# Performance work log

Measured on AMD Instinct MI355X. Metric: run time of the kernel, lower is better.

Reference implementation:

```python
import jax, jax.numpy as jnp
import numpy as np

B, CIN, COUT, H, W = 4, 128, 128, 128, 128
K, G, PAD = 3, 4, 1  # kernel_size, deformable_groups, padding=(K-1)//2
CG = CIN // G


def setup_inputs() -> dict:
    key = jax.random.key(0)
    k1, k2, k3, k4 = jax.random.split(key, 4)
    x = jax.random.normal(k1, (B, CIN, H, W), jnp.float32)
    # 1x1 offset conv (in module it is zero-initialized; use small random values
    # so the bilinear-sampling path is actually exercised)
    w_off = jax.random.normal(k2, (G * K * K * 2, CIN), jnp.float32) * 0.01
    b_off = jax.random.normal(k3, (G * K * K * 2,), jnp.float32) * 0.1
    # DeformConv weight [Cout, Cin, K, K] (DCNv1 has no bias)
    w_def = jax.random.normal(k4, (COUT, CIN, K, K), jnp.float32) * (1.0 / np.sqrt(CIN * K * K))
    return {"x": x, "w_off": w_off, "b_off": b_off, "w_def": w_def}


def _deform_conv(x, offset, w):
    """DCNv1: per-location bilinear gather at offset positions, then weighted sum.

    x:      [B, CIN, H, W]
    offset: [B, G*K*K*2, H, W], channel layout (g, kk, {dy,dx})
    w:      [COUT, CIN, K, K]
    """
    off = offset.reshape(B, G, K * K, 2, H, W)
    ky, kx = np.meshgrid(np.arange(K), np.arange(K), indexing='ij')
    ky = jnp.asarray(ky.reshape(-1), jnp.float32)
    kx = jnp.asarray(kx.reshape(-1), jnp.float32)
    # sampling positions: p = p0 + p_k - pad + offset   -> [B, G, K*K, H, W]
    py = off[:, :, :, 0] + (ky - PAD).reshape(1, 1, K * K, 1, 1) \
         + jnp.arange(H, dtype=jnp.float32).reshape(1, 1, 1, H, 1)
    px = off[:, :, :, 1] + (kx - PAD).reshape(1, 1, K * K, 1, 1) \
         + jnp.arange(W, dtype=jnp.float32).reshape(1, 1, 1, 1, W)

    y0 = jnp.floor(py)
    x0 = jnp.floor(px)
    wy1 = py - y0
    wx1 = px - x0
    wy0 = 1.0 - wy1
    wx0 = 1.0 - wx1
    y0i = y0.astype(jnp.int32)
    x0i = x0.astype(jnp.int32)

    xg = x.reshape(B, G, CG, H * W)  # grouped channels for gather

    def gather(yi, xi):
        # zero padding outside the feature map (mmcv DeformConv semantics)
        valid = (yi >= 0) & (yi < H) & (xi >= 0) & (xi < W)
        idx = (jnp.clip(yi, 0, H - 1) * W + jnp.clip(xi, 0, W - 1)).reshape(B, G, 1, K * K * H * W)
        v = jnp.take_along_axis(xg, idx, axis=3).reshape(B, G, CG, K * K, H, W)
        return v * valid[:, :, None].astype(x.dtype)

    # accumulate the four bilinear corners sequentially to bound peak memory
    val = gather(y0i, x0i) * (wy0 * wx0)[:, :, None]
    val = val + gather(y0i, x0i + 1) * (wy0 * wx1)[:, :, None]
    val = val + gather(y0i + 1, x0i) * (wy1 * wx0)[:, :, None]
    val = val + gather(y0i + 1, x0i + 1) * (wy1 * wx1)[:, :, None]

    wg = w.reshape(COUT, G, CG, K * K)
    return jnp.einsum('bgckhw,ogck->bohw', val, wg)


def reference(x, w_off, b_off, w_def):
    # 1x1 offset conv with bias
    offset = jnp.einsum('bchw,oc->bohw', x, w_off) + b_off[None, :, None, None]
    return jax.nn.relu(_deform_conv(x, offset, w_def))
```

## Files before the change

### kernel.cpp

```cpp
#include <hip/hip_runtime.h>
#include <hip/hip_fp16.h>


#define HW 16384

typedef _Float16 h2 __attribute__((ext_vector_type(2)));
typedef _Float16 h8 __attribute__((ext_vector_type(8)));
typedef float floatx4 __attribute__((ext_vector_type(4)));

static __device__ __forceinline__ unsigned pkrtz(float a, float b) {
  auto h = __builtin_amdgcn_cvt_pkrtz(a, b);
  return __builtin_bit_cast(unsigned, h);
}
static __device__ __forceinline__ h2 u2h2(unsigned u) { return __builtin_bit_cast(h2, u); }
static __device__ __forceinline__ unsigned h2u(h2 h) { return __builtin_bit_cast(unsigned, h); }
static __device__ __forceinline__ h2 splat_lo(unsigned u) {
  unsigned v = (u & 0xffffu) | (u << 16); return u2h2(v);
}
static __device__ __forceinline__ h2 splat_hi(unsigned u) {
  unsigned v = (u >> 16) | (u & 0xffff0000u); return u2h2(v);
}

__global__ __launch_bounds__(256) void prep_w(
    const float* __restrict__ w_off, const float* __restrict__ w_def,
    _Float16* __restrict__ woff, _Float16* __restrict__ wdef) {
  int idx = blockIdx.x * 256 + threadIdx.x;
  int stride = gridDim.x * 256;
  for (int i = idx; i < 147456; i += stride) {
    int j = i & 7, l = (i >> 3) & 63, ot = (i >> 9) & 7, ks = (i >> 12) & 3, kk = i >> 14;
    int o = ot * 16 + (l & 15);
    int c = ks * 32 + ((l >> 4) << 3) + j;
    wdef[i] = (_Float16)w_def[(o * 128 + c) * 9 + kk];
  }
  for (int i = idx; i < 10240; i += stride) {
    int j = i & 7, l = (i >> 3) & 63, t = i >> 9;
    int mt = t % 5, ks = t / 5;
    int o = mt * 16 + (l & 15);
    int c = ks * 32 + ((l >> 4) << 3) + j;
    woff[i] = (o < 72) ? (_Float16)w_off[o * 128 + c] : (_Float16)0.f;
  }
}

__global__ __launch_bounds__(256) void prep_row(
    const float* __restrict__ x, const _Float16* __restrict__ woff,
    const float* __restrict__ b_off, unsigned* __restrict__ offs2,
    _Float16* __restrict__ x16) {
  __shared__ uint2 xpk[32 * 128];
  int tid = threadIdx.x, lane = tid & 63, wv = tid >> 6;
  int i = blockIdx.x;
  int L = (i & 7) * 64 + (i >> 3);
  int b = L >> 7, h = L & 127;

#pragma unroll
  for (int it = 0; it < 4; it++) {
    int u = it * 256 + tid;
    int px4 = u & 31, cqq = u >> 5;
    const float* xp = x + (((size_t)b * 128 + cqq * 4) * 128 + h) * 128 + px4 * 4;
    float4 v0 = *(const float4*)xp;
    float4 v1 = *(const float4*)(xp + HW);
    float4 v2 = *(const float4*)(xp + 2 * HW);
    float4 v3 = *(const float4*)(xp + 3 * HW);
    uint2* dst = &xpk[cqq * 128 + px4 * 4];
    uint2 w;
    w.x = pkrtz(v0.x, v1.x); w.y = pkrtz(v2.x, v3.x); dst[0] = w;
    w.x = pkrtz(v0.y, v1.y); w.y = pkrtz(v2.y, v3.y); dst[1] = w;
    w.x = pkrtz(v0.z, v1.z); w.y = pkrtz(v2.z, v3.z); dst[2] = w;
    w.x = pkrtz(v0.w, v1.w); w.y = pkrtz(v2.w, v3.w); dst[3] = w;
  }
  __syncthreads();

  uint4* xrow = (uint4*)(x16 + (((size_t)b * 128 + h) * 128) * 128);
#pragma unroll
  for (int it = 0; it < 8; it++) {
    int u = it * 256 + tid;
    int oct = u & 15, px = u >> 4;
    uint2 a = xpk[(2 * oct) * 128 + px];
    uint2 c = xpk[(2 * oct + 1) * 128 + px];
    uint4 qv; qv.x = a.x; qv.y = a.y; qv.z = c.x; qv.w = c.y;
    xrow[px * 16 + oct] = qv;
  }

  floatx4 acc[5][2];
#pragma unroll
  for (int mt = 0; mt < 5; mt++) { acc[mt][0] = (floatx4)0.f; acc[mt][1] = (floatx4)0.f; }
  const h8* A = (const h8*)woff;
  int q = lane >> 4, col = lane & 15;
#pragma unroll
  for (int ks = 0; ks < 4; ks++) {
    h8 av[5];
#pragma unroll
    for (int mt = 0; mt < 5; mt++) av[mt] = A[(ks * 5 + mt) * 64 + lane];
#pragma unroll
    for (int nn = 0; nn < 2; nn++) {
      int pxl = (2 * wv + nn) * 16 + col;
      uint2 lo = xpk[(ks * 8 + 2 * q) * 128 + pxl];
      uint2 hi = xpk[(ks * 8 + 2 * q + 1) * 128 + pxl];
      uint4 qq; qq.x = lo.x; qq.y = lo.y; qq.z = hi.x; qq.w = hi.y;
      h8 bv = __builtin_bit_cast(h8, qq);
#pragma unroll
      for (int mt = 0; mt < 5; mt++)
        acc[mt][nn] = __builtin_amdgcn_mfma_f32_16x16x32_f16(av[mt], bv, acc[mt][nn], 0, 0, 0);
    }
  }
#pragma unroll
  for (int mt = 0; mt < 5; mt++) {
    if (mt == 4 && q >= 2) continue;
    int o0 = mt * 16 + q * 4;
    float4 bo = *(const float4*)(b_off + o0);
#pragma unroll
    for (int nn = 0; nn < 2; nn++) {
      floatx4 f = acc[mt][nn];
      int pp = (2 * wv + nn) * 16 + col;
      unsigned* dst = offs2 + ((size_t)b * 36 + (o0 >> 1)) * HW + h * 128 + pp;
      dst[0]  = pkrtz(f[0] + bo.x, f[1] + bo.y);
      dst[HW] = pkrtz(f[2] + bo.z, f[3] + bo.w);
    }
  }
}

__global__ __launch_bounds__(256, 2) void deform_conv(
    const _Float16* __restrict__ x16, const _Float16* __restrict__ wdef,
    const unsigned* __restrict__ offs2, float* __restrict__ out) {
  __shared__ uint4 xs[5 * 136 * 5];

  int tid = threadIdx.x, lane = tid & 63, wv = tid >> 6;
  int i = blockIdx.x;
  int L = (i & 7) * 64 + (i >> 3);
  int b = L >> 7, h = L & 127;
  int rlo = min(max(h - 2, 0), 123);
  int pa = 32 * wv + (lane & 15);
  int q = lane >> 4;

  floatx4 acc[2][8];
#pragma unroll
  for (int f = 0; f < 2; f++)
#pragma unroll
    for (int ot = 0; ot < 8; ot++) acc[f][ot] = (floatx4)0.f;

  for (int t = 0; t < 4; t++) {
    __syncthreads();
    unsigned dd[9][2];
#pragma unroll
    for (int kk = 0; kk < 9; kk++)
#pragma unroll
      for (int f = 0; f < 2; f++)
        dd[kk][f] = offs2[((size_t)b * 36 + t * 9 + kk) * HW + h * 128 + pa + 16 * f];
#pragma unroll
    for (int it = 0; it < 11; it++) {
      int u = tid + it * 256;
      if (u < 2720) {
        int oct = u & 3, v2 = u >> 2;
        int px = v2 % 136, r = v2 / 136;
        int pc = min(max(px - 4, 0), 127);
        const uint4* src = (const uint4*)(x16 + (((size_t)b * 128 + rlo + r) * 128 + pc) * 128 + t * 32) + oct;
        xs[(r * 136 + px) * 5 + oct] = *src;
      }
    }
    __syncthreads();

#pragma unroll
    for (int kk = 0; kk < 9; kk++) {
      const uint4* Ak = (const uint4*)wdef + (size_t)(kk * 2048 + t * 512);
      h8 av[8];
#pragma unroll
      for (int ot = 0; ot < 8; ot++) av[ot] = __builtin_bit_cast(h8, Ak[ot * 64 + lane]);
#pragma unroll
      for (int f = 0; f < 2; f++) {
        int p = pa + 16 * f;
        h2 d = u2h2(dd[kk][f]);
        float dy = (float)d[0], dx = (float)d[1];
        float py = (float)h + (float)(kk / 3 - 1) + dy;
        float pxs = (float)p + (float)(kk % 3 - 1) + dx;
        float y0f = floorf(py), x0f = floorf(pxs);
        int y0 = (int)y0f, x0 = (int)x0f;
        float wy1f = py - y0f, wx1 = pxs - x0f;
        float wy0f = 1.f - wy1f, wx0 = 1.f - wx1;
        int x1 = x0 + 1, y1 = y0 + 1;
        int xb = min(max(x0, 0), 126);
        float fx0 = (x0 >= 0 && x0 <= 127) ? 1.f : 0.f;
        float fx1 = (x1 >= 0 && x1 <= 127) ? 1.f : 0.f;
        float wAf = (x0 == xb ? wx0 * fx0 : 0.f) + (x1 == xb ? wx1 * fx1 : 0.f);
        float wBf = (x0 == xb + 1 ? wx0 * fx0 : 0.f) + (x1 == xb + 1 ? wx1 * fx1 : 0.f);
        float fy0 = (y0 >= 0 && y0 <= 127) ? 1.f : 0.f;
        float fy1 = (y1 >= 0 && y1 <= 127) ? 1.f : 0.f;
        int r0 = min(max(min(max(y0, 0), 127) - rlo, 0), 4);
        int r1 = min(max(min(max(y1, 0), 127) - rlo, 0), 4);
        int lx = xb + 4;
        unsigned wy_pk = pkrtz(wy0f * fy0, wy1f * fy1);
        unsigned wab_pk = pkrtz(wAf, wBf);

        int i0 = (r0 * 136 + lx) * 5 + q;
        int i1 = (r1 * 136 + lx) * 5 + q;
        uint4 P = xs[i0], Q = xs[i0 + 5], R = xs[i1], S = xs[i1 + 5];
        h2 wy0 = splat_lo(wy_pk), wy1 = splat_hi(wy_pk);
        h2 wA = splat_lo(wab_pk), wB = splat_hi(wab_pk);
        uint4 bq;
        bq.x = h2u(wy0 * (wA * u2h2(P.x) + wB * u2h2(Q.x)) + wy1 * (wA * u2h2(R.x) + wB * u2h2(S.x)));
        bq.y = h2u(wy0 * (wA * u2h2(P.y) + wB * u2h2(Q.y)) + wy1 * (wA * u2h2(R.y) + wB * u2h2(S.y)));
        bq.z = h2u(wy0 * (wA * u2h2(P.z) + wB * u2h2(Q.z)) + wy1 * (wA * u2h2(R.z) + wB * u2h2(S.z)));
        bq.w = h2u(wy0 * (wA * u2h2(P.w) + wB * u2h2(Q.w)) + wy1 * (wA * u2h2(R.w) + wB * u2h2(S.w)));
        h8 bv = __builtin_bit_cast(h8, bq);
#pragma unroll
        for (int ot = 0; ot < 8; ot++)
          acc[f][ot] = __builtin_amdgcn_mfma_f32_16x16x32_f16(av[ot], bv, acc[f][ot], 0, 0, 0);
      }
    }
  }

#pragma unroll
  for (int f = 0; f < 2; f++) {
    float* ob = out + (size_t)b * 128 * HW + h * 128 + pa + 16 * f;
#pragma unroll
    for (int ot = 0; ot < 8; ot++) {
      floatx4 fv = acc[f][ot];
#pragma unroll
      for (int reg = 0; reg < 4; reg++) {
        int o = ot * 16 + q * 4 + reg;
        ob[(size_t)o * HW] = fmaxf(fv[reg], 0.f);
      }
    }
  }
}

extern "C" void kernel_launch(void* const* d_in, const int* in_sizes, int n_in,
                              void* d_out, int out_size, void* d_ws, size_t ws_size,
                              hipStream_t stream) {
  const float* x     = (const float*)d_in[0];
  const float* w_off = (const float*)d_in[1];
  const float* b_off = (const float*)d_in[2];
  const float* w_def = (const float*)d_in[3];
  float* out = (float*)d_out;

  _Float16* wdef = (_Float16*)d_ws;
  _Float16* woff = (_Float16*)((char*)d_ws + 294912);
  unsigned* offs2 = (unsigned*)((char*)d_ws + 315392);
  _Float16* x16  = (_Float16*)((char*)d_ws + 9752576);

  prep_w<<<dim3(288), dim3(256), 0, stream>>>(w_off, w_def, woff, wdef);
  prep_row<<<dim3(512), dim3(256), 0, stream>>>(x, woff, b_off, offs2, x16);
  deform_conv<<<dim3(512), dim3(256), 0, stream>>>(x16, wdef, offs2, out);
}
```

Before: 136.6 us.

## Split prep_row into half-rows, trim deform LDS halo, fold bilinear weights

prep_row now handles half a row per block (1024 blocks) with half the LDS and accumulators. deform_conv drops the 136-wide padded halo tile for a 128-wide one, which removes the bounds check and modulo in the load loop, and raises launch bounds to 3 blocks per CU. The bilinear blend now uses four precomputed corner weights instead of nested separable products, which cuts half-precision ops. Relies on xb being clamped to 0..126 so no halo is needed, and fp16 rounding of the product weights changes slightly.

```diff
diff --git a/kernel.cpp b/kernel.cpp
--- a/kernel.cpp
+++ b/kernel.cpp
@@ -45,22 +45,23 @@
     const float* __restrict__ x, const _Float16* __restrict__ woff,
     const float* __restrict__ b_off, unsigned* __restrict__ offs2,
     _Float16* __restrict__ x16) {
-  __shared__ uint2 xpk[32 * 128];
+  __shared__ uint2 xpk[32 * 64];
   int tid = threadIdx.x, lane = tid & 63, wv = tid >> 6;
   int i = blockIdx.x;
-  int L = (i & 7) * 64 + (i >> 3);
-  int b = L >> 7, h = L & 127;
-
-#pragma unroll
-  for (int it = 0; it < 4; it++) {
+  int L = (i & 7) * 128 + (i >> 3);
+  int half = L & 1, h = (L >> 1) & 127, b = L >> 8;
+  int p0 = half * 64;
+
+#pragma unroll
+  for (int it = 0; it < 2; it++) {
     int u = it * 256 + tid;
-    int px4 = u & 31, cqq = u >> 5;
-    const float* xp = x + (((size_t)b * 128 + cqq * 4) * 128 + h) * 128 + px4 * 4;
+    int px4 = u & 15, cqq = u >> 4;
+    const float* xp = x + (((size_t)b * 128 + cqq * 4) * 128 + h) * 128 + p0 + px4 * 4;
     float4 v0 = *(const float4*)xp;
     float4 v1 = *(const float4*)(xp + HW);
     float4 v2 = *(const float4*)(xp + 2 * HW);
     float4 v3 = *(const float4*)(xp + 3 * HW);
-    uint2* dst = &xpk[cqq * 128 + px4 * 4];
+    uint2* dst = &xpk[cqq * 64 + px4 * 4];
     uint2 w;
     w.x = pkrtz(v0.x, v1.x); w.y = pkrtz(v2.x, v3.x); dst[0] = w;
     w.x = pkrtz(v0.y, v1.y); w.y = pkrtz(v2.y, v3.y); dst[1] = w;
@@ -69,59 +70,49 @@
   }
   __syncthreads();
 
-  uint4* xrow = (uint4*)(x16 + (((size_t)b * 128 + h) * 128) * 128);
-#pragma unroll
-  for (int it = 0; it < 8; it++) {
+  uint4* xrow = (uint4*)(x16 + (((size_t)b * 128 + h) * 128 + p0) * 128);
+#pragma unroll
+  for (int it = 0; it < 4; it++) {
     int u = it * 256 + tid;
     int oct = u & 15, px = u >> 4;
-    uint2 a = xpk[(2 * oct) * 128 + px];
-    uint2 c = xpk[(2 * oct + 1) * 128 + px];
+    uint2 a = xpk[(2 * oct) * 64 + px];
+    uint2 c = xpk[(2 * oct + 1) * 64 + px];
     uint4 qv; qv.x = a.x; qv.y = a.y; qv.z = c.x; qv.w = c.y;
     xrow[px * 16 + oct] = qv;
   }
 
-  floatx4 acc[5][2];
-#pragma unroll
-  for (int mt = 0; mt < 5; mt++) { acc[mt][0] = (floatx4)0.f; acc[mt][1] = (floatx4)0.f; }
+  floatx4 acc[5];
+#pragma unroll
+  for (int mt = 0; mt < 5; mt++) acc[mt] = (floatx4)0.f;
   const h8* A = (const h8*)woff;
   int q = lane >> 4, col = lane & 15;
+  int pxl = wv * 16 + col;
 #pragma unroll
   for (int ks = 0; ks < 4; ks++) {
-    h8 av[5];
-#pragma unroll
-    for (int mt = 0; mt < 5; mt++) av[mt] = A[(ks * 5 + mt) * 64 + lane];
-#pragma unroll
-    for (int nn = 0; nn < 2; nn++) {
-      int pxl = (2 * wv + nn) * 16 + col;
-      uint2 lo = xpk[(ks * 8 + 2 * q) * 128 + pxl];
-      uint2 hi = xpk[(ks * 8 + 2 * q + 1) * 128 + pxl];
-      uint4 qq; qq.x = lo.x; qq.y = lo.y; qq.z = hi.x; qq.w = hi.y;
-      h8 bv = __builtin_bit_cast(h8, qq);
-#pragma unroll
-      for (int mt = 0; mt < 5; mt++)
-        acc[mt][nn] = __builtin_amdgcn_mfma_f32_16x16x32_f16(av[mt], bv, acc[mt][nn], 0, 0, 0);
-    }
+    uint2 lo = xpk[(ks * 8 + 2 * q) * 64 + pxl];
+    uint2 hi = xpk[(ks * 8 + 2 * q + 1) * 64 + pxl];
+    uint4 qq; qq.x = lo.x; qq.y = lo.y; qq.z = hi.x; qq.w = hi.y;
+    h8 bv = __builtin_bit_cast(h8, qq);
+#pragma unroll
+    for (int mt = 0; mt < 5; mt++)
+      acc[mt] = __builtin_amdgcn_mfma_f32_16x16x32_f16(A[(ks * 5 + mt) * 64 + lane], bv, acc[mt], 0, 0, 0);
   }
 #pragma unroll
   for (int mt = 0; mt < 5; mt++) {
     if (mt == 4 && q >= 2) continue;
     int o0 = mt * 16 + q * 4;
     float4 bo = *(const float4*)(b_off + o0);
-#pragma unroll
-    for (int nn = 0; nn < 2; nn++) {
-      floatx4 f = acc[mt][nn];
-      int pp = (2 * wv + nn) * 16 + col;
-      unsigned* dst = offs2 + ((size_t)b * 36 + (o0 >> 1)) * HW + h * 128 + pp;
-      dst[0]  = pkrtz(f[0] + bo.x, f[1] + bo.y);
-      dst[HW] = pkrtz(f[2] + bo.z, f[3] + bo.w);
-    }
-  }
-}
-
-__global__ __launch_bounds__(256, 2) void deform_conv(
+    floatx4 f = acc[mt];
+    unsigned* dst = offs2 + ((size_t)b * 36 + (o0 >> 1)) * HW + h * 128 + p0 + pxl;
+    dst[0]  = pkrtz(f[0] + bo.x, f[1] + bo.y);
+    dst[HW] = pkrtz(f[2] + bo.z, f[3] + bo.w);
+  }
+}
+
+__global__ __launch_bounds__(256, 3) void deform_conv(
     const _Float16* __restrict__ x16, const _Float16* __restrict__ wdef,
     const unsigned* __restrict__ offs2, float* __restrict__ out) {
-  __shared__ uint4 xs[5 * 136 * 5];
+  __shared__ uint4 xs[5 * 128 * 5];
 
   int tid = threadIdx.x, lane = tid & 63, wv = tid >> 6;
   int i = blockIdx.x;
@@ -146,15 +137,12 @@
       for (int f = 0; f < 2; f++)
         dd[kk][f] = offs2[((size_t)b * 36 + t * 9 + kk) * HW + h * 128 + pa + 16 * f];
 #pragma unroll
-    for (int it = 0; it < 11; it++) {
+    for (int it = 0; it < 10; it++) {
       int u = tid + it * 256;
-      if (u < 2720) {
-        int oct = u & 3, v2 = u >> 2;
-        int px = v2 % 136, r = v2 / 136;
-        int pc = min(max(px - 4, 0), 127);
-        const uint4* src = (const uint4*)(x16 + (((size_t)b * 128 + rlo + r) * 128 + pc) * 128 + t * 32) + oct;
-        xs[(r * 136 + px) * 5 + oct] = *src;
-      }
+      int oct = u & 3, v2 = u >> 2;
+      int px = v2 & 127, r = v2 >> 7;
+      const uint4* src = (const uint4*)(x16 + (((size_t)b * 128 + rlo + r) * 128 + px) * 128 + t * 32) + oct;
+      xs[(r * 128 + px) * 5 + oct] = *src;
     }
     __syncthreads();
 
@@ -185,20 +173,20 @@
         float fy1 = (y1 >= 0 && y1 <= 127) ? 1.f : 0.f;
         int r0 = min(max(min(max(y0, 0), 127) - rlo, 0), 4);
         int r1 = min(max(min(max(y1, 0), 127) - rlo, 0), 4);
-        int lx = xb + 4;
-        unsigned wy_pk = pkrtz(wy0f * fy0, wy1f * fy1);
-        unsigned wab_pk = pkrtz(wAf, wBf);
-
-        int i0 = (r0 * 136 + lx) * 5 + q;
-        int i1 = (r1 * 136 + lx) * 5 + q;
+        float wy0e = wy0f * fy0, wy1e = wy1f * fy1;
+        unsigned w0_pk = pkrtz(wy0e * wAf, wy0e * wBf);
+        unsigned w1_pk = pkrtz(wy1e * wAf, wy1e * wBf);
+
+        int i0 = (r0 * 128 + xb) * 5 + q;
+        int i1 = (r1 * 128 + xb) * 5 + q;
         uint4 P = xs[i0], Q = xs[i0 + 5], R = xs[i1], S = xs[i1 + 5];
-        h2 wy0 = splat_lo(wy_pk), wy1 = splat_hi(wy_pk);
-        h2 wA = splat_lo(wab_pk), wB = splat_hi(wab_pk);
+        h2 w00 = splat_lo(w0_pk), w01 = splat_hi(w0_pk);
+        h2 w10 = splat_lo(w1_pk), w11 = splat_hi(w1_pk);
         uint4 bq;
-        bq.x = h2u(wy0 * (wA * u2h2(P.x) + wB * u2h2(Q.x)) + wy1 * (wA * u2h2(R.x) + wB * u2h2(S.x)));
-        bq.y = h2u(wy0 * (wA * u2h2(P.y) + wB * u2h2(Q.y)) + wy1 * (wA * u2h2(R.y) + wB * u2h2(S.y)));
-        bq.z = h2u(wy0 * (wA * u2h2(P.z) + wB * u2h2(Q.z)) + wy1 * (wA * u2h2(R.z) + wB * u2h2(S.z)));
-        bq.w = h2u(wy0 * (wA * u2h2(P.w) + wB * u2h2(Q.w)) + wy1 * (wA * u2h2(R.w) + wB * u2h2(S.w)));
+        bq.x = h2u(w00 * u2h2(P.x) + w01 * u2h2(Q.x) + w10 * u2h2(R.x) + w11 * u2h2(S.x));
+        bq.y = h2u(w00 * u2h2(P.y) + w01 * u2h2(Q.y) + w10 * u2h2(R.y) + w11 * u2h2(S.y));
+        bq.z = h2u(w00 * u2h2(P.z) + w01 * u2h2(Q.z) + w10 * u2h2(R.z) + w11 * u2h2(S.z));
+        bq.w = h2u(w00 * u2h2(P.w) + w01 * u2h2(Q.w) + w10 * u2h2(R.w) + w11 * u2h2(S.w));
         h8 bv = __builtin_bit_cast(h8, bq);
 #pragma unroll
         for (int ot = 0; ot < 8; ot++)
@@ -237,6 +225,6 @@
   _Float16* x16  = (_Float16*)((char*)d_ws + 9752576);
 
   prep_w<<<dim3(288), dim3(256), 0, stream>>>(w_off, w_def, woff, wdef);
-  prep_row<<<dim3(512), dim3(256), 0, stream>>>(x, woff, b_off, offs2, x16);
+  prep_row<<<dim3(1024), dim3(256), 0, stream>>>(x, woff, b_off, offs2, x16);
   deform_conv<<<dim3(512), dim3(256), 0, stream>>>(x16, wdef, offs2, out);
 }
```

Result: slower. 153.3 us (+12.2%).
